# Performance work log

Hardware: AMD Instinct MI355X
Metric: run time of the kernel (lower is better)

The kernel has to match this reference:

```python
import jax, jax.numpy as jnp
import numpy as np

TMP1 = 0.01
TMP2 = 0.1
TMP3 = 0.1
NEG_MARGIN = 0.1  # referenced in source forward but never set in __init__; fixed here
CLAMP_MAX = 88.0


def setup_inputs() -> dict:
    key = jax.random.key(0)
    scores = jax.random.normal(key, (512, 8192), dtype=jnp.float32)
    k_vals = jnp.array([1, 5, 10], dtype=jnp.int32)
    return {"scores": scores, "k_vals": k_vals, "pos_num": 16}


def reference(scores, k_vals, pos_num):
    # scores: [B, N]; first `pos_num` columns are positives (gt == 1), rest negatives.
    P = pos_num
    K = k_vals.shape[0]
    pos = scores[:, :P]          # [B, P]
    neg = scores[:, P:]          # [B, N-P]

    # pairwise diffs: pos rows and neg rows of the per-sample [N, P] diff matrix
    pos_diff = pos[:, :, None] - pos[:, None, :]                    # [B, P, P]
    neg_diff = neg[:, :, None] - pos[:, None, :] + NEG_MARGIN       # [B, N-P, P]

    # negative rows: soft step via temperature-scaled softplus, two-sided
    neg_term = jnp.where(
        neg_diff >= 0,
        jnp.logaddexp(0.0, neg_diff / TMP2) + 0.1,
        jnp.logaddexp(0.0, neg_diff / TMP1),
    )                                                               # [B, N-P, P]

    # positive rows: hard indicator (detached in source), zero the diagonal
    eye = jnp.eye(P, dtype=scores.dtype)
    pos_term = (pos_diff >= 0).astype(scores.dtype) * (1.0 - eye)   # [B, P, P]

    # soft rank of each positive: 1 + sum over all rows
    rank = 1.0 + pos_term.sum(axis=1) + neg_term.sum(axis=1)        # [B, P]

    # soft recall@k penalty per positive and cutoff
    z = (rank[:, :, None] - k_vals[None, None, :].astype(scores.dtype)) / TMP3
    recall = jnp.logaddexp(0.0, jnp.minimum(z, CLAMP_MAX))          # [B, P, K]

    per_sample = recall.sum(axis=(1, 2)) / (P * K)                  # [B]
    return per_sample.mean()
```

## Files before the change

kernel.cpp:

```cpp
#include <hip/hip_runtime.h>


#define ROWS 512
#define COLS 8192
#define POSN 16
#define NK 3
#define NCHUNK 4
#define CHUNK_F4 511

typedef float f32x4 __attribute__((ext_vector_type(4)));

__global__ __launch_bounds__(256, 6)
void negsum_kernel(const float* __restrict__ scores, float* __restrict__ ws)
{
    const int b     = blockIdx.x;
    const int row   = b >> 2;
    const int chunk = b & 3;
    const int wave  = threadIdx.x >> 6;
    const int lane  = threadIdx.x & 63;
    const float* rowp = scores + (size_t)row * COLS;

    const float C10 = 14.4269504089f;
    const float A0  = 1.44269504089f;
    const float LN2 = 0.69314718055994531f;

    float p10[4];
#pragma unroll
    for (int jj = 0; jj < 4; ++jj)
        p10[jj] = rowp[wave * 4 + jj] * C10;

    const f32x4* negs =
        reinterpret_cast<const f32x4*>(rowp + POSN) + (size_t)chunk * CHUNK_F4;

    f32x4 v[8];
#pragma unroll
    for (int it = 0; it < 8; ++it) {
        int f = it * 64 + lane;
        if (f > CHUNK_F4 - 1) f = CHUNK_F4 - 1;
        v[it] = negs[f];
    }
    if (lane == 63) {
        v[7].x = -1.0e30f; v[7].y = -1.0e30f; v[7].z = -1.0e30f; v[7].w = -1.0e30f;
    }

    float prod[4] = {1.f, 1.f, 1.f, 1.f};
    float accM[4] = {0.f, 0.f, 0.f, 0.f};
    int   ncnt[4] = {0, 0, 0, 0};

#pragma unroll
    for (int it = 0; it < 8; ++it) {
        float a10[4];
        a10[0] = __fmaf_rn(v[it].x, C10, A0);
        a10[1] = __fmaf_rn(v[it].y, C10, A0);
        a10[2] = __fmaf_rn(v[it].z, C10, A0);
        a10[3] = __fmaf_rn(v[it].w, C10, A0);
#pragma unroll
        for (int e = 0; e < 4; ++e) {
#pragma unroll
            for (int jj = 0; jj < 4; ++jj) {
                const float t   = a10[e] - p10[jj];
                const float arg = fminf(-t, 10.0f * t);
                const float u   = __builtin_amdgcn_exp2f(arg);
                prod[jj] = __fmaf_rn(prod[jj], u, prod[jj]);
                accM[jj] += fmaxf(t, 0.0f);
                ncnt[jj] += (int)(__float_as_uint(t) >> 31);
            }
        }
    }

#pragma unroll
    for (int jj = 0; jj < 4; ++jj) {
        const float nge = 32.0f - (float)ncnt[jj];
        float s = __fmaf_rn(accM[jj] + __builtin_amdgcn_logf(prod[jj]),
                            LN2, 0.1f * nge);
#pragma unroll
        for (int off = 32; off > 0; off >>= 1)
            s += __shfl_xor(s, off);
        if (lane == 0)
            ws[((size_t)(chunk * ROWS + row)) * POSN + wave * 4 + jj] = s;
    }
}

__global__ __launch_bounds__(256)
void finalize_kernel(const float* __restrict__ scores,
                     const float* __restrict__ ws,
                     const int* __restrict__ k_vals,
                     float* __restrict__ out)
{
    const int gid = blockIdx.x * 256 + threadIdx.x;
    const int row = gid >> 4;
    const int j   = gid & 15;
    const float* rowp = scores + (size_t)row * COLS;

    float negsum = 0.0f;
#pragma unroll
    for (int c = 0; c < NCHUNK; ++c)
        negsum += ws[((size_t)(c * ROWS + row)) * POSN + j];

    const float pj = rowp[j];
    float cnt = -1.0f;
#pragma unroll
    for (int i = 0; i < POSN; ++i)
        cnt += (rowp[i] >= pj) ? 1.0f : 0.0f;

    const float rank = 1.0f + cnt + negsum;

    float rsum = 0.0f;
#pragma unroll
    for (int k = 0; k < NK; ++k) {
        float z = (rank - (float)k_vals[k]) * 10.0f;
        z = fminf(z, 88.0f);
        const float e2 = __builtin_amdgcn_exp2f(-1.44269504089f * fabsf(z));
        rsum += fmaxf(z, 0.0f)
              + 0.69314718056f * __builtin_amdgcn_logf(1.0f + e2);
    }

    const int wave = threadIdx.x >> 6;
    const int lane = threadIdx.x & 63;
#pragma unroll
    for (int off = 32; off > 0; off >>= 1)
        rsum += __shfl_xor(rsum, off);

    __shared__ float sp[4];
    if (lane == 0) sp[wave] = rsum;
    __syncthreads();
    if (threadIdx.x == 0) {
        const float s = sp[0] + sp[1] + sp[2] + sp[3];
        atomicAdd(out, s * (1.0f / ((float)POSN * (float)NK * (float)ROWS)));
    }
}

extern "C" void kernel_launch(void* const* d_in, const int* in_sizes, int n_in,
                              void* d_out, int out_size, void* d_ws, size_t ws_size,
                              hipStream_t stream) {
    const float* scores = (const float*)d_in[0];
    const int*   k_vals = (const int*)d_in[1];
    float* out = (float*)d_out;
    float* ws  = (float*)d_ws;

    hipMemsetAsync(out, 0, sizeof(float), stream);
    negsum_kernel<<<ROWS * NCHUNK, 256, 0, stream>>>(scores, ws);
    finalize_kernel<<<(ROWS * POSN) / 256, 256, 0, stream>>>(scores, ws, k_vals, out);
}
```

Baseline: 83.72 us.

## Split negatives across waves so each wave handles all positives

Reassigns work in the negative-sum kernel. Each wave now covers a distinct quarter of the chunk's negatives against all 16 positives, instead of every wave reloading the whole chunk for 4 positives. This removes the 4x redundant loads, which now use nontemporal hints, and gives each lane 16 independent accumulation chains. The count of non-negative differences moves from per-lane shift/add to a wave ballot plus popcount. The cost is higher register pressure (occupancy hint lowered to 5) and a 4x larger workspace that the finalize kernel must sum per wave.

```diff
diff --git a/kernel.cpp b/kernel.cpp
--- a/kernel.cpp
+++ b/kernel.cpp
@@ -10,7 +10,7 @@
 
 typedef float f32x4 __attribute__((ext_vector_type(4)));
 
-__global__ __launch_bounds__(256, 6)
+__global__ __launch_bounds__(256, 5)
 void negsum_kernel(const float* __restrict__ scores, float* __restrict__ ws)
 {
     const int b     = blockIdx.x;
@@ -24,31 +24,37 @@
     const float A0  = 1.44269504089f;
     const float LN2 = 0.69314718055994531f;
 
-    float p10[4];
+    float p10[POSN];
 #pragma unroll
-    for (int jj = 0; jj < 4; ++jj)
-        p10[jj] = rowp[wave * 4 + jj] * C10;
+    for (int j = 0; j < POSN; ++j)
+        p10[j] = rowp[j] * C10;
 
     const f32x4* negs =
         reinterpret_cast<const f32x4*>(rowp + POSN) + (size_t)chunk * CHUNK_F4;
 
-    f32x4 v[8];
+    f32x4 v[2];
+    bool valid[2];
 #pragma unroll
-    for (int it = 0; it < 8; ++it) {
-        int f = it * 64 + lane;
-        if (f > CHUNK_F4 - 1) f = CHUNK_F4 - 1;
-        v[it] = negs[f];
+    for (int it = 0; it < 2; ++it) {
+        int f = wave * 128 + it * 64 + lane;
+        valid[it] = (f < CHUNK_F4);
+        v[it] = __builtin_nontemporal_load(negs + (valid[it] ? f : CHUNK_F4 - 1));
     }
-    if (lane == 63) {
-        v[7].x = -1.0e30f; v[7].y = -1.0e30f; v[7].z = -1.0e30f; v[7].w = -1.0e30f;
+#pragma unroll
+    for (int it = 0; it < 2; ++it) {
+        if (!valid[it]) {
+            v[it].x = -1.0e30f; v[it].y = -1.0e30f;
+            v[it].z = -1.0e30f; v[it].w = -1.0e30f;
+        }
     }
 
-    float prod[4] = {1.f, 1.f, 1.f, 1.f};
-    float accM[4] = {0.f, 0.f, 0.f, 0.f};
-    int   ncnt[4] = {0, 0, 0, 0};
+    float prod[POSN], accM[POSN];
+    int   nge[POSN];
+#pragma unroll
+    for (int j = 0; j < POSN; ++j) { prod[j] = 1.0f; accM[j] = 0.0f; nge[j] = 0; }
 
 #pragma unroll
-    for (int it = 0; it < 8; ++it) {
+    for (int it = 0; it < 2; ++it) {
         float a10[4];
         a10[0] = __fmaf_rn(v[it].x, C10, A0);
         a10[1] = __fmaf_rn(v[it].y, C10, A0);
@@ -57,27 +63,27 @@
 #pragma unroll
         for (int e = 0; e < 4; ++e) {
 #pragma unroll
-            for (int jj = 0; jj < 4; ++jj) {
-                const float t   = a10[e] - p10[jj];
+            for (int j = 0; j < POSN; ++j) {
+                const float t   = a10[e] - p10[j];
                 const float arg = fminf(-t, 10.0f * t);
                 const float u   = __builtin_amdgcn_exp2f(arg);
-                prod[jj] = __fmaf_rn(prod[jj], u, prod[jj]);
-                accM[jj] += fmaxf(t, 0.0f);
-                ncnt[jj] += (int)(__float_as_uint(t) >> 31);
+                prod[j] = __fmaf_rn(prod[j], u, prod[j]);
+                accM[j] += fmaxf(t, 0.0f);
+                nge[j] += (int)__popcll(__ballot(t >= 0.0f));
             }
         }
     }
 
 #pragma unroll
-    for (int jj = 0; jj < 4; ++jj) {
-        const float nge = 32.0f - (float)ncnt[jj];
-        float s = __fmaf_rn(accM[jj] + __builtin_amdgcn_logf(prod[jj]),
-                            LN2, 0.1f * nge);
+    for (int j = 0; j < POSN; ++j) {
+        float s = accM[j] + __builtin_amdgcn_logf(prod[j]);
 #pragma unroll
         for (int off = 32; off > 0; off >>= 1)
             s += __shfl_xor(s, off);
-        if (lane == 0)
-            ws[((size_t)(chunk * ROWS + row)) * POSN + wave * 4 + jj] = s;
+        if (lane == 0) {
+            s = __fmaf_rn(s, LN2, 0.1f * (float)nge[j]);
+            ws[(((size_t)chunk * ROWS + row) * POSN + j) * 4 + wave] = s;
+        }
     }
 }
 
@@ -95,7 +101,9 @@
     float negsum = 0.0f;
 #pragma unroll
     for (int c = 0; c < NCHUNK; ++c)
-        negsum += ws[((size_t)(c * ROWS + row)) * POSN + j];
+#pragma unroll
+        for (int w = 0; w < 4; ++w)
+            negsum += ws[(((size_t)c * ROWS + row) * POSN + j) * 4 + w];
 
     const float pj = rowp[j];
     float cnt = -1.0f;
```

Measured after the change: 111.5 us. 33.2% more time.
